# Kernel optimization log

Hardware: AMD Instinct MI355X
Metric: run time of the kernel (lower is better)

Reference implementation:

```python
import jax, jax.numpy as jnp
import numpy as np

B, L, D = 16, 2048, 64

def setup_inputs() -> dict:
    key = jax.random.key(0)
    kq, kk, kv = jax.random.split(key, 3)
    q = jax.random.normal(kq, (B, L, D), dtype=jnp.float32)
    k = jax.random.normal(kk, (B, L, D), dtype=jnp.float32)
    v = jax.random.normal(kv, (B, L, D), dtype=jnp.float32)
    return {"q": q, "k": k, "v": v}

def reference(q, k, v):
    # scores: [B, L_q, L_k] = q @ k^T  (no scale applied, faithful to source)
    scores = jnp.einsum("bqd,bkd->bqk", q, k)
    attention = jax.nn.softmax(scores, axis=2)
    # dropout p=0.0 -> identity
    # source returns (v, attention), NOT the context
    return (v, attention)
```

## Files before the change

### kernel.cpp

```cpp
#include <hip/hip_runtime.h>
#include <hip/hip_bf16.h>

typedef short s16x8 __attribute__((ext_vector_type(8)));
typedef float f32x4 __attribute__((ext_vector_type(4)));

#define B_ 16
#define L_ 2048
#define D_ 64
#define V_ELEMS (B_ * L_ * D_)

__device__ __forceinline__ unsigned rne1(float f) {
    unsigned u = __builtin_bit_cast(unsigned, f);
    return (u + 0x7FFFu + ((u >> 16) & 1u)) >> 16;
}
__device__ __forceinline__ unsigned pack2(float a, float b) {
    return (rne1(a) & 0xFFFFu) | (rne1(b) << 16);
}

__device__ __forceinline__ void split8(float4 a, float4 b, s16x8& hi, s16x8& lo) {
    float f[8] = {a.x, a.y, a.z, a.w, b.x, b.y, b.z, b.w};
    s16x8 h, l;
#pragma unroll
    for (int i = 0; i < 8; ++i) {
        unsigned u = __builtin_bit_cast(unsigned, f[i]);
        h[i] = (short)(u >> 16);
        float lf = f[i] - __builtin_bit_cast(float, u & 0xFFFF0000u);
        l[i] = (short)rne1(lf);
    }
    hi = h; lo = l;
}

__global__ void copy_v_kernel(const float4* __restrict__ v, float4* __restrict__ o) {
    int i = blockIdx.x * blockDim.x + threadIdx.x;
    o[i] = v[i];
}

__global__ void prep_qk_kernel(const float4* __restrict__ q, const float4* __restrict__ k,
                               uint2* __restrict__ qhi, uint2* __restrict__ qlo,
                               uint2* __restrict__ khi, uint2* __restrict__ klo) {
    int i = blockIdx.x * blockDim.x + threadIdx.x;
    float4 fq = q[i];
    float4 fk = k[i];
    unsigned u0 = __builtin_bit_cast(unsigned, fq.x), u1 = __builtin_bit_cast(unsigned, fq.y);
    unsigned u2 = __builtin_bit_cast(unsigned, fq.z), u3 = __builtin_bit_cast(unsigned, fq.w);
    qhi[i] = make_uint2((u0 >> 16) | (u1 & 0xFFFF0000u), (u2 >> 16) | (u3 & 0xFFFF0000u));
    qlo[i] = make_uint2(
        pack2(fq.x - __builtin_bit_cast(float, u0 & 0xFFFF0000u),
              fq.y - __builtin_bit_cast(float, u1 & 0xFFFF0000u)),
        pack2(fq.z - __builtin_bit_cast(float, u2 & 0xFFFF0000u),
              fq.w - __builtin_bit_cast(float, u3 & 0xFFFF0000u)));
    u0 = __builtin_bit_cast(unsigned, fk.x); u1 = __builtin_bit_cast(unsigned, fk.y);
    u2 = __builtin_bit_cast(unsigned, fk.z); u3 = __builtin_bit_cast(unsigned, fk.w);
    khi[i] = make_uint2((u0 >> 16) | (u1 & 0xFFFF0000u), (u2 >> 16) | (u3 & 0xFFFF0000u));
    klo[i] = make_uint2(
        pack2(fk.x - __builtin_bit_cast(float, u0 & 0xFFFF0000u),
              fk.y - __builtin_bit_cast(float, u1 & 0xFFFF0000u)),
        pack2(fk.z - __builtin_bit_cast(float, u2 & 0xFFFF0000u),
              fk.w - __builtin_bit_cast(float, u3 & 0xFFFF0000u)));
}

__device__ __forceinline__ void store4f(float* p, unsigned u0, unsigned u1, float inv) {
    float4 w;
    w.x = __builtin_bit_cast(float, u0 << 16) * inv;
    w.y = __builtin_bit_cast(float, u0 & 0xFFFF0000u) * inv;
    w.z = __builtin_bit_cast(float, u1 << 16) * inv;
    w.w = __builtin_bit_cast(float, u1 & 0xFFFF0000u) * inv;
    *(float4*)p = w;
}

template <bool PRE>
__global__ __launch_bounds__(256, 2) void attn_kernel(
    const float* __restrict__ qf, const float* __restrict__ kf,
    const ushort* __restrict__ qhi, const ushort* __restrict__ qlo,
    const ushort* __restrict__ khi, const ushort* __restrict__ klo,
    float* __restrict__ og) {
    const int b    = blockIdx.x >> 6;
    const int q0   = (blockIdx.x & 63) << 5;
    const int tid  = threadIdx.x;
    const int wave = tid >> 6;
    const int lane = tid & 63;
    const int nq   = lane & 15;
    const int quad = lane >> 4;

    s16x8 bhi[2][2], blo[2][2];
#pragma unroll
    for (int t = 0; t < 2; ++t) {
        const size_t off = ((size_t)(b * L_ + q0 + t * 16 + nq)) * D_ + quad * 8;
        if constexpr (PRE) {
            bhi[t][0] = *(const s16x8*)(qhi + off);
            bhi[t][1] = *(const s16x8*)(qhi + off + 32);
            blo[t][0] = *(const s16x8*)(qlo + off);
            blo[t][1] = *(const s16x8*)(qlo + off + 32);
        } else {
            float4 a0 = *(const float4*)(qf + off), a1 = *(const float4*)(qf + off + 4);
            float4 a2 = *(const float4*)(qf + off + 32), a3 = *(const float4*)(qf + off + 36);
            split8(a0, a1, bhi[t][0], blo[t][0]);
            split8(a2, a3, bhi[t][1], blo[t][1]);
        }
    }

    const size_t krow0 = (size_t)b * L_ + (size_t)wave * 512 + nq;
    float s0 = 0.0f, s1 = 0.0f;
    unsigned pk0[64], pk1[64];

#pragma unroll
    for (int t = 0; t < 32; ++t) {
        const size_t off = (krow0 + (size_t)t * 16) * D_ + quad * 8;
        s16x8 ahi0, ahi1, alo0, alo1;
        if constexpr (PRE) {
            ahi0 = *(const s16x8*)(khi + off);
            ahi1 = *(const s16x8*)(khi + off + 32);
            alo0 = *(const s16x8*)(klo + off);
            alo1 = *(const s16x8*)(klo + off + 32);
        } else {
            float4 a0 = *(const float4*)(kf + off), a1 = *(const float4*)(kf + off + 4);
            float4 a2 = *(const float4*)(kf + off + 32), a3 = *(const float4*)(kf + off + 36);
            split8(a0, a1, ahi0, alo0);
            split8(a2, a3, ahi1, alo1);
        }
        f32x4 c0 = {0.f, 0.f, 0.f, 0.f}, c1 = {0.f, 0.f, 0.f, 0.f};
        c0 = __builtin_amdgcn_mfma_f32_16x16x32_bf16(ahi0, bhi[0][0], c0, 0, 0, 0);
        c0 = __builtin_amdgcn_mfma_f32_16x16x32_bf16(ahi1, bhi[0][1], c0, 0, 0, 0);
        c0 = __builtin_amdgcn_mfma_f32_16x16x32_bf16(ahi0, blo[0][0], c0, 0, 0, 0);
        c0 = __builtin_amdgcn_mfma_f32_16x16x32_bf16(ahi1, blo[0][1], c0, 0, 0, 0);
        c0 = __builtin_amdgcn_mfma_f32_16x16x32_bf16(alo0, bhi[0][0], c0, 0, 0, 0);
        c0 = __builtin_amdgcn_mfma_f32_16x16x32_bf16(alo1, bhi[0][1], c0, 0, 0, 0);
        c1 = __builtin_amdgcn_mfma_f32_16x16x32_bf16(ahi0, bhi[1][0], c1, 0, 0, 0);
        c1 = __builtin_amdgcn_mfma_f32_16x16x32_bf16(ahi1, bhi[1][1], c1, 0, 0, 0);
        c1 = __builtin_amdgcn_mfma_f32_16x16x32_bf16(ahi0, blo[1][0], c1, 0, 0, 0);
        c1 = __builtin_amdgcn_mfma_f32_16x16x32_bf16(ahi1, blo[1][1], c1, 0, 0, 0);
        c1 = __builtin_amdgcn_mfma_f32_16x16x32_bf16(alo0, bhi[1][0], c1, 0, 0, 0);
        c1 = __builtin_amdgcn_mfma_f32_16x16x32_bf16(alo1, bhi[1][1], c1, 0, 0, 0);
        float e0 = __expf(c0[0]), e1 = __expf(c0[1]), e2 = __expf(c0[2]), e3 = __expf(c0[3]);
        s0 += (e0 + e1) + (e2 + e3);
        pk0[2 * t]     = pack2(e0, e1);
        pk0[2 * t + 1] = pack2(e2, e3);
        float g0 = __expf(c1[0]), g1 = __expf(c1[1]), g2 = __expf(c1[2]), g3 = __expf(c1[3]);
        s1 += (g0 + g1) + (g2 + g3);
        pk1[2 * t]     = pack2(g0, g1);
        pk1[2 * t + 1] = pack2(g2, g3);
    }

    s0 += __shfl_xor(s0, 16); s0 += __shfl_xor(s0, 32);
    s1 += __shfl_xor(s1, 16); s1 += __shfl_xor(s1, 32);
    __shared__ float wsum[4][2][16];
    if (lane < 16) { wsum[wave][0][lane] = s0; wsum[wave][1][lane] = s1; }
    __syncthreads();
    const float inv0 = 1.0f / ((wsum[0][0][nq] + wsum[1][0][nq]) + (wsum[2][0][nq] + wsum[3][0][nq]));
    const float inv1 = 1.0f / ((wsum[0][1][nq] + wsum[1][1][nq]) + (wsum[2][1][nq] + wsum[3][1][nq]));

    float* op0 = og + ((size_t)(b * L_ + q0 + nq)) * L_ + wave * 512 + quad * 4;
    float* op1 = op0 + (size_t)16 * L_;
#pragma unroll
    for (int t = 0; t < 32; ++t) {
        store4f(op0, pk0[2 * t], pk0[2 * t + 1], inv0); op0 += 16;
        store4f(op1, pk1[2 * t], pk1[2 * t + 1], inv1); op1 += 16;
    }
}

extern "C" void kernel_launch(void* const* d_in, const int* in_sizes, int n_in,
                              void* d_out, int out_size, void* d_ws, size_t ws_size,
                              hipStream_t stream) {
    const float* q = (const float*)d_in[0];
    const float* k = (const float*)d_in[1];
    const float* v = (const float*)d_in[2];
    float* out = (float*)d_out;

    copy_v_kernel<<<dim3(V_ELEMS / 4 / 256), dim3(256), 0, stream>>>(
        (const float4*)v, (float4*)out);

    float* att = out + (size_t)V_ELEMS;
    const size_t plane = (size_t)V_ELEMS;
    const size_t need  = 4 * plane * sizeof(ushort);
    ushort* qhi = (ushort*)d_ws;
    ushort* qlo = qhi + plane;
    ushort* khi = qlo + plane;
    ushort* klo = khi + plane;

    if (ws_size >= need) {
        prep_qk_kernel<<<dim3(V_ELEMS / 4 / 256), dim3(256), 0, stream>>>(
            (const float4*)q, (const float4*)k,
            (uint2*)qhi, (uint2*)qlo, (uint2*)khi, (uint2*)klo);
        attn_kernel<true><<<dim3(B_ * (L_ / 32)), dim3(256), 0, stream>>>(
            q, k, qhi, qlo, khi, klo, att);
    } else {
        attn_kernel<false><<<dim3(B_ * (L_ / 32)), dim3(256), 0, stream>>>(
            q, k, qhi, qlo, khi, klo, att);
    }
}
```

Measured before the change: 383.9 us.

## Recompute scores in store pass to drop register cache and raise occupancy

Removes the 128-register per-thread cache of packed exp values by recomputing QK^T scores and exp in a second pass during output stores, which lets launch bounds rise from 2 to 4 blocks per CU. Also fuses the V copy into the Q/K split prep kernel, swizzles block indices across batches, and uses nontemporal stores for the attention output. The cost is doubling the MFMA and exp work and re-reading K from workspace. Output precision also changes, since stores now write full fp32 exp instead of bf16-rounded values.

```diff
diff --git a/kernel.cpp b/kernel.cpp
--- a/kernel.cpp
+++ b/kernel.cpp
@@ -8,6 +8,7 @@
 #define L_ 2048
 #define D_ 64
 #define V_ELEMS (B_ * L_ * D_)
+#define MFMA16 __builtin_amdgcn_mfma_f32_16x16x32_bf16
 
 __device__ __forceinline__ unsigned rne1(float f) {
     unsigned u = __builtin_bit_cast(unsigned, f);
@@ -35,10 +36,13 @@
     o[i] = v[i];
 }
 
-__global__ void prep_qk_kernel(const float4* __restrict__ q, const float4* __restrict__ k,
-                               uint2* __restrict__ qhi, uint2* __restrict__ qlo,
-                               uint2* __restrict__ khi, uint2* __restrict__ klo) {
+__global__ void prep_qkv_kernel(const float4* __restrict__ q, const float4* __restrict__ k,
+                                const float4* __restrict__ v,
+                                uint2* __restrict__ qhi, uint2* __restrict__ qlo,
+                                uint2* __restrict__ khi, uint2* __restrict__ klo,
+                                float4* __restrict__ o) {
     int i = blockIdx.x * blockDim.x + threadIdx.x;
+    o[i] = v[i];
     float4 fq = q[i];
     float4 fk = k[i];
     unsigned u0 = __builtin_bit_cast(unsigned, fq.x), u1 = __builtin_bit_cast(unsigned, fq.y);
@@ -59,23 +63,49 @@
               fk.w - __builtin_bit_cast(float, u3 & 0xFFFF0000u)));
 }
 
-__device__ __forceinline__ void store4f(float* p, unsigned u0, unsigned u1, float inv) {
-    float4 w;
-    w.x = __builtin_bit_cast(float, u0 << 16) * inv;
-    w.y = __builtin_bit_cast(float, u0 & 0xFFFF0000u) * inv;
-    w.z = __builtin_bit_cast(float, u1 << 16) * inv;
-    w.w = __builtin_bit_cast(float, u1 & 0xFFFF0000u) * inv;
-    *(float4*)p = w;
+template <bool PRE>
+__device__ __forceinline__ void score_tile(
+    const float* __restrict__ kf, const ushort* __restrict__ khi,
+    const ushort* __restrict__ klo, size_t off,
+    const s16x8 (&bhi)[2][2], const s16x8 (&blo)[2][2],
+    f32x4& c0, f32x4& c1) {
+    s16x8 ahi0, ahi1, alo0, alo1;
+    if constexpr (PRE) {
+        ahi0 = *(const s16x8*)(khi + off);
+        ahi1 = *(const s16x8*)(khi + off + 32);
+        alo0 = *(const s16x8*)(klo + off);
+        alo1 = *(const s16x8*)(klo + off + 32);
+    } else {
+        float4 a0 = *(const float4*)(kf + off), a1 = *(const float4*)(kf + off + 4);
+        float4 a2 = *(const float4*)(kf + off + 32), a3 = *(const float4*)(kf + off + 36);
+        split8(a0, a1, ahi0, alo0);
+        split8(a2, a3, ahi1, alo1);
+    }
+    c0 = (f32x4){0.f, 0.f, 0.f, 0.f};
+    c1 = (f32x4){0.f, 0.f, 0.f, 0.f};
+    c0 = MFMA16(ahi0, bhi[0][0], c0, 0, 0, 0);
+    c0 = MFMA16(ahi1, bhi[0][1], c0, 0, 0, 0);
+    c0 = MFMA16(ahi0, blo[0][0], c0, 0, 0, 0);
+    c0 = MFMA16(ahi1, blo[0][1], c0, 0, 0, 0);
+    c0 = MFMA16(alo0, bhi[0][0], c0, 0, 0, 0);
+    c0 = MFMA16(alo1, bhi[0][1], c0, 0, 0, 0);
+    c1 = MFMA16(ahi0, bhi[1][0], c1, 0, 0, 0);
+    c1 = MFMA16(ahi1, bhi[1][1], c1, 0, 0, 0);
+    c1 = MFMA16(ahi0, blo[1][0], c1, 0, 0, 0);
+    c1 = MFMA16(ahi1, blo[1][1], c1, 0, 0, 0);
+    c1 = MFMA16(alo0, bhi[1][0], c1, 0, 0, 0);
+    c1 = MFMA16(alo1, bhi[1][1], c1, 0, 0, 0);
 }
 
 template <bool PRE>
-__global__ __launch_bounds__(256, 2) void attn_kernel(
+__global__ __launch_bounds__(256, 4) void attn_kernel(
     const float* __restrict__ qf, const float* __restrict__ kf,
     const ushort* __restrict__ qhi, const ushort* __restrict__ qlo,
     const ushort* __restrict__ khi, const ushort* __restrict__ klo,
     float* __restrict__ og) {
-    const int b    = blockIdx.x >> 6;
-    const int q0   = (blockIdx.x & 63) << 5;
+    const int bid  = ((blockIdx.x & 7) << 7) | (blockIdx.x >> 3);
+    const int b    = bid >> 6;
+    const int q0   = (bid & 63) << 5;
     const int tid  = threadIdx.x;
     const int wave = tid >> 6;
     const int lane = tid & 63;
@@ -100,45 +130,15 @@
     }
 
     const size_t krow0 = (size_t)b * L_ + (size_t)wave * 512 + nq;
+
     float s0 = 0.0f, s1 = 0.0f;
-    unsigned pk0[64], pk1[64];
-
-#pragma unroll
+#pragma unroll 2
     for (int t = 0; t < 32; ++t) {
         const size_t off = (krow0 + (size_t)t * 16) * D_ + quad * 8;
-        s16x8 ahi0, ahi1, alo0, alo1;
-        if constexpr (PRE) {
-            ahi0 = *(const s16x8*)(khi + off);
-            ahi1 = *(const s16x8*)(khi + off + 32);
-            alo0 = *(const s16x8*)(klo + off);
-            alo1 = *(const s16x8*)(klo + off + 32);
-        } else {
-            float4 a0 = *(const float4*)(kf + off), a1 = *(const float4*)(kf + off + 4);
-            float4 a2 = *(const float4*)(kf + off + 32), a3 = *(const float4*)(kf + off + 36);
-            split8(a0, a1, ahi0, alo0);
-            split8(a2, a3, ahi1, alo1);
-        }
-        f32x4 c0 = {0.f, 0.f, 0.f, 0.f}, c1 = {0.f, 0.f, 0.f, 0.f};
-        c0 = __builtin_amdgcn_mfma_f32_16x16x32_bf16(ahi0, bhi[0][0], c0, 0, 0, 0);
-        c0 = __builtin_amdgcn_mfma_f32_16x16x32_bf16(ahi1, bhi[0][1], c0, 0, 0, 0);
-        c0 = __builtin_amdgcn_mfma_f32_16x16x32_bf16(ahi0, blo[0][0], c0, 0, 0, 0);
-        c0 = __builtin_amdgcn_mfma_f32_16x16x32_bf16(ahi1, blo[0][1], c0, 0, 0, 0);
-        c0 = __builtin_amdgcn_mfma_f32_16x16x32_bf16(alo0, bhi[0][0], c0, 0, 0, 0);
-        c0 = __builtin_amdgcn_mfma_f32_16x16x32_bf16(alo1, bhi[0][1], c0, 0, 0, 0);
-        c1 = __builtin_amdgcn_mfma_f32_16x16x32_bf16(ahi0, bhi[1][0], c1, 0, 0, 0);
-        c1 = __builtin_amdgcn_mfma_f32_16x16x32_bf16(ahi1, bhi[1][1], c1, 0, 0, 0);
-        c1 = __builtin_amdgcn_mfma_f32_16x16x32_bf16(ahi0, blo[1][0], c1, 0, 0, 0);
-        c1 = __builtin_amdgcn_mfma_f32_16x16x32_bf16(ahi1, blo[1][1], c1, 0, 0, 0);
-        c1 = __builtin_amdgcn_mfma_f32_16x16x32_bf16(alo0, bhi[1][0], c1, 0, 0, 0);
-        c1 = __builtin_amdgcn_mfma_f32_16x16x32_bf16(alo1, bhi[1][1], c1, 0, 0, 0);
-        float e0 = __expf(c0[0]), e1 = __expf(c0[1]), e2 = __expf(c0[2]), e3 = __expf(c0[3]);
-        s0 += (e0 + e1) + (e2 + e3);
-        pk0[2 * t]     = pack2(e0, e1);
-        pk0[2 * t + 1] = pack2(e2, e3);
-        float g0 = __expf(c1[0]), g1 = __expf(c1[1]), g2 = __expf(c1[2]), g3 = __expf(c1[3]);
-        s1 += (g0 + g1) + (g2 + g3);
-        pk1[2 * t]     = pack2(g0, g1);
-        pk1[2 * t + 1] = pack2(g2, g3);
+        f32x4 c0, c1;
+        score_tile<PRE>(kf, khi, klo, off, bhi, blo, c0, c1);
+        s0 += (__expf(c0[0]) + __expf(c0[1])) + (__expf(c0[2]) + __expf(c0[3]));
+        s1 += (__expf(c1[0]) + __expf(c1[1])) + (__expf(c1[2]) + __expf(c1[3]));
     }
 
     s0 += __shfl_xor(s0, 16); s0 += __shfl_xor(s0, 32);
@@ -151,10 +151,18 @@
 
     float* op0 = og + ((size_t)(b * L_ + q0 + nq)) * L_ + wave * 512 + quad * 4;
     float* op1 = op0 + (size_t)16 * L_;
-#pragma unroll
+#pragma unroll 2
     for (int t = 0; t < 32; ++t) {
-        store4f(op0, pk0[2 * t], pk0[2 * t + 1], inv0); op0 += 16;
-        store4f(op1, pk1[2 * t], pk1[2 * t + 1], inv1); op1 += 16;
+        const size_t off = (krow0 + (size_t)t * 16) * D_ + quad * 8;
+        f32x4 c0, c1;
+        score_tile<PRE>(kf, khi, klo, off, bhi, blo, c0, c1);
+        f32x4 w0, w1;
+        w0[0] = __expf(c0[0]) * inv0; w0[1] = __expf(c0[1]) * inv0;
+        w0[2] = __expf(c0[2]) * inv0; w0[3] = __expf(c0[3]) * inv0;
+        w1[0] = __expf(c1[0]) * inv1; w1[1] = __expf(c1[1]) * inv1;
+        w1[2] = __expf(c1[2]) * inv1; w1[3] = __expf(c1[3]) * inv1;
+        __builtin_nontemporal_store(w0, (f32x4*)(op0 + (size_t)t * 16));
+        __builtin_nontemporal_store(w1, (f32x4*)(op1 + (size_t)t * 16));
     }
 }
 
@@ -166,9 +174,6 @@
     const float* v = (const float*)d_in[2];
     float* out = (float*)d_out;
 
-    copy_v_kernel<<<dim3(V_ELEMS / 4 / 256), dim3(256), 0, stream>>>(
-        (const float4*)v, (float4*)out);
-
     float* att = out + (size_t)V_ELEMS;
     const size_t plane = (size_t)V_ELEMS;
     const size_t need  = 4 * plane * sizeof(ushort);
@@ -178,12 +183,14 @@
     ushort* klo = khi + plane;
 
     if (ws_size >= need) {
-        prep_qk_kernel<<<dim3(V_ELEMS / 4 / 256), dim3(256), 0, stream>>>(
-            (const float4*)q, (const float4*)k,
-            (uint2*)qhi, (uint2*)qlo, (uint2*)khi, (uint2*)klo);
+        prep_qkv_kernel<<<dim3(V_ELEMS / 4 / 256), dim3(256), 0, stream>>>(
+            (const float4*)q, (const float4*)k, (const float4*)v,
+            (uint2*)qhi, (uint2*)qlo, (uint2*)khi, (uint2*)klo, (float4*)out);
         attn_kernel<true><<<dim3(B_ * (L_ / 32)), dim3(256), 0, stream>>>(
             q, k, qhi, qlo, khi, klo, att);
     } else {
+        copy_v_kernel<<<dim3(V_ELEMS / 4 / 256), dim3(256), 0, stream>>>(
+            (const float4*)v, (float4*)out);
         attn_kernel<false><<<dim3(B_ * (L_ / 32)), dim3(256), 0, stream>>>(
             q, k, qhi, qlo, khi, klo, att);
     }
```

After: 389.4 us. No clear change (+1.4%).
